# Optimization experiments

Measured on AMD Instinct MI355X. Metric: run time of the kernel, lower is better.

The kernel has to match this reference:

```python
import jax, jax.numpy as jnp
import numpy as np

B = 8192
N_IN = 1024
N_OUT = 1024
IN_OUT = N_IN + N_OUT


def setup_inputs() -> dict:
    key = jax.random.key(0)
    ks = jax.random.split(key, 11)
    s = 1.0 / np.sqrt(IN_OUT)  # nn.Linear default init scale
    inp = {
        "x": jax.random.normal(ks[0], (B, N_IN), dtype=jnp.float32),
        "out_tm1": jax.random.normal(ks[1], (B, N_OUT), dtype=jnp.float32),
        "state_tm1": jax.random.normal(ks[2], (B, N_OUT), dtype=jnp.float32),
        "Wf": jax.random.uniform(ks[3], (IN_OUT, N_OUT), jnp.float32, -s, s),
        "bf": jax.random.uniform(ks[4], (N_OUT,), jnp.float32, -s, s),
        "Wi": jax.random.uniform(ks[5], (IN_OUT, N_OUT), jnp.float32, -s, s),
        "bi": jax.random.uniform(ks[6], (N_OUT,), jnp.float32, -s, s),
        "Wc": jax.random.uniform(ks[7], (IN_OUT, N_OUT), jnp.float32, -s, s),
        "bc": jax.random.uniform(ks[8], (N_OUT,), jnp.float32, -s, s),
        "Wo": jax.random.uniform(ks[9], (IN_OUT, N_OUT), jnp.float32, -s, s),
        "bo": jax.random.uniform(ks[10], (N_OUT,), jnp.float32, -s, s),
    }
    return inp


def reference(x, out_tm1, state_tm1, Wf, bf, Wi, bi, Wc, bc, Wo, bo):
    xh = jnp.concatenate((x, out_tm1), axis=-1)  # [B, n_in+n_out]
    f = jax.nn.sigmoid(xh @ Wf + bf)             # forget gate
    i = jax.nn.sigmoid(xh @ Wi + bi)             # input gate
    c = jnp.tanh(xh @ Wc + bc)                   # candidates
    o = jax.nn.sigmoid(xh @ Wo + bo)             # output gate
    new_state = state_tm1 * f + i * c
    output_t = o * jnp.tanh(new_state)
    return (output_t, new_state)
```

## Files before the change

### kernel.cpp

```cpp
#include <hip/hip_runtime.h>

#define B_DIM 8192
#define NIN   1024
#define NOUT  1024
#define KDIM  2048

#define BM 128
#define BN 64
#define BK 64

typedef __bf16 bf16x8 __attribute__((ext_vector_type(8)));
typedef float  f32x4  __attribute__((ext_vector_type(4)));

__device__ __forceinline__ unsigned short f2bf(float f) {
  unsigned int u = __float_as_uint(f);
  u += 0x7fff + ((u >> 16) & 1);
  return (unsigned short)(u >> 16);
}

__device__ __forceinline__ float sigmoid_f(float x) {
  return 1.0f / (1.0f + __expf(-x));
}
__device__ __forceinline__ float tanh_f(float x) {
  return 1.0f - 2.0f / (__expf(2.0f * x) + 1.0f);
}

__device__ __forceinline__ void gload_lds16(const void* g, void* l) {
  __builtin_amdgcn_global_load_lds(
      (const __attribute__((address_space(1))) void*)g,
      (__attribute__((address_space(3))) void*)l, 16, 0, 0);
}

__global__ void pack_xh_kernel(const float* __restrict__ x,
                               const float* __restrict__ h,
                               unsigned short* __restrict__ xh) {
  const long total = (long)B_DIM * KDIM / 4;
  for (long i = (long)blockIdx.x * blockDim.x + threadIdx.x; i < total;
       i += (long)gridDim.x * blockDim.x) {
    long e = i * 4;
    int b = (int)(e >> 11);
    int c = (int)(e & 2047);
    float4 v = (c < NIN)
        ? *reinterpret_cast<const float4*>(x + (long)b * NIN + c)
        : *reinterpret_cast<const float4*>(h + (long)b * NOUT + (c - NIN));
    ushort4 o;
    o.x = f2bf(v.x); o.y = f2bf(v.y); o.z = f2bf(v.z); o.w = f2bf(v.w);
    *reinterpret_cast<ushort4*>(xh + e) = o;
  }
}

__global__ void transpose_w_kernel(const float* __restrict__ Wf,
                                   const float* __restrict__ Wi,
                                   const float* __restrict__ Wc,
                                   const float* __restrict__ Wo,
                                   unsigned short* __restrict__ wt) {
  __shared__ float tile[32][33];
  const int g = blockIdx.z;
  const float* W = (g == 0) ? Wf : (g == 1) ? Wi : (g == 2) ? Wc : Wo;
  const int n0 = blockIdx.x * 32;
  const int k0 = blockIdx.y * 32;
  const int tx = threadIdx.x, ty = threadIdx.y;
#pragma unroll
  for (int r = ty; r < 32; r += 8)
    tile[r][tx] = W[(long)(k0 + r) * NOUT + n0 + tx];
  __syncthreads();
  unsigned short* dst = wt + (long)g * NOUT * KDIM;
#pragma unroll
  for (int r = ty; r < 32; r += 8)
    dst[(long)(n0 + r) * KDIM + k0 + tx] = f2bf(tile[tx][r]);
}

__global__ __launch_bounds__(256, 2)
void lstm_gemm_kernel(const unsigned short* __restrict__ xh,
                      const unsigned short* __restrict__ wt,
                      const float* __restrict__ state,
                      const float* __restrict__ bfp,
                      const float* __restrict__ bip,
                      const float* __restrict__ bcp,
                      const float* __restrict__ bop,
                      float* __restrict__ out) {
  __shared__ __attribute__((aligned(16))) unsigned short lds_a[BM * BK];
  __shared__ __attribute__((aligned(16))) unsigned short lds_b[4][BN * BK];

  const int tid  = threadIdx.x;
  const int wave = tid >> 6;
  const int lane = tid & 63;
  const int m0 = blockIdx.y * BM;
  const int n0 = blockIdx.x * BN;
  const int wm = wave >> 1;
  const int wn = wave & 1;

  f32x4 acc[4][2][4];
#pragma unroll
  for (int mi = 0; mi < 4; ++mi)
#pragma unroll
    for (int ni = 0; ni < 2; ++ni)
#pragma unroll
      for (int g = 0; g < 4; ++g)
        acc[mi][ni][g] = (f32x4){0.f, 0.f, 0.f, 0.f};

  const char* xh_b = (const char*)xh;
  const char* wt_b = (const char*)wt;

  for (int kt = 0; kt < KDIM / BK; ++kt) {
#pragma unroll
    for (int j = 0; j < 4; ++j) {
      int off  = (wave * 4 + j) * 1024 + lane * 16;
      int row  = off >> 7;
      int colb = off & 127;
      gload_lds16(xh_b + ((long)(m0 + row) * 4096 + kt * 128 + colb),
                  (char*)lds_a + (wave * 4 + j) * 1024);
    }
#pragma unroll
    for (int j = 0; j < 8; ++j) {
      int off  = j * 1024 + lane * 16;
      int row  = off >> 7;
      int colb = off & 127;
      gload_lds16(wt_b + ((long)wave * 4194304 +
                          (long)(n0 + row) * 4096 + kt * 128 + colb),
                  (char*)lds_b + wave * 8192 + j * 1024);
    }
    __syncthreads();

#pragma unroll
    for (int s = 0; s < 2; ++s) {
      const int kb = s * 32 + (lane >> 4) * 8;
      bf16x8 af[4];
#pragma unroll
      for (int mi = 0; mi < 4; ++mi)
        af[mi] = *reinterpret_cast<const bf16x8*>(
            lds_a + (wm * 64 + mi * 16 + (lane & 15)) * BK + kb);
#pragma unroll
      for (int g = 0; g < 4; ++g) {
#pragma unroll
        for (int ni = 0; ni < 2; ++ni) {
          bf16x8 bfr = *reinterpret_cast<const bf16x8*>(
              lds_b[g] + (wn * 32 + ni * 16 + (lane & 15)) * BK + kb);
#pragma unroll
          for (int mi = 0; mi < 4; ++mi)
            acc[mi][ni][g] = __builtin_amdgcn_mfma_f32_16x16x32_bf16(
                af[mi], bfr, acc[mi][ni][g], 0, 0, 0);
        }
      }
    }
    __syncthreads();
  }

  const int colbase = n0 + wn * 32 + (lane & 15);
  const int rowbase = m0 + wm * 64 + ((lane >> 4) << 2);
#pragma unroll
  for (int ni = 0; ni < 2; ++ni) {
    const int c = colbase + ni * 16;
    const float bfv = bfp[c], biv = bip[c], bcv = bcp[c], bov = bop[c];
#pragma unroll
    for (int mi = 0; mi < 4; ++mi) {
      const int r0 = rowbase + mi * 16;
#pragma unroll
      for (int r = 0; r < 4; ++r) {
        const long row = r0 + r;
        float fg = sigmoid_f(acc[mi][ni][0][r] + bfv);
        float ig = sigmoid_f(acc[mi][ni][1][r] + biv);
        float cg = tanh_f(acc[mi][ni][2][r] + bcv);
        float og = sigmoid_f(acc[mi][ni][3][r] + bov);
        float st = state[row * NOUT + c];
        float ns = st * fg + ig * cg;
        out[row * NOUT + c] = og * tanh_f(ns);
        out[(long)B_DIM * NOUT + row * NOUT + c] = ns;
      }
    }
  }
}

extern "C" void kernel_launch(void* const* d_in, const int* in_sizes, int n_in,
                              void* d_out, int out_size, void* d_ws, size_t ws_size,
                              hipStream_t stream) {
  const float* x     = (const float*)d_in[0];
  const float* h     = (const float*)d_in[1];
  const float* state = (const float*)d_in[2];
  const float* Wf    = (const float*)d_in[3];
  const float* bfp   = (const float*)d_in[4];
  const float* Wi    = (const float*)d_in[5];
  const float* bip   = (const float*)d_in[6];
  const float* Wc    = (const float*)d_in[7];
  const float* bcp   = (const float*)d_in[8];
  const float* Wo    = (const float*)d_in[9];
  const float* bop   = (const float*)d_in[10];
  float* out = (float*)d_out;

  unsigned short* xh = (unsigned short*)d_ws;
  unsigned short* wt = (unsigned short*)((char*)d_ws +
                        (size_t)B_DIM * KDIM * 2);

  hipLaunchKernelGGL(pack_xh_kernel, dim3(2048), dim3(256), 0, stream,
                     x, h, xh);
  hipLaunchKernelGGL(transpose_w_kernel, dim3(NOUT / 32, KDIM / 32, 4),
                     dim3(32, 8), 0, stream, Wf, Wi, Wc, Wo, wt);
  hipLaunchKernelGGL(lstm_gemm_kernel, dim3(NOUT / BN, B_DIM / BM),
                     dim3(256), 0, stream,
                     xh, wt, state, bfp, bip, bcp, bop, out);
}
```

Measured before the change: 179.5 us.

## Rewrite LSTM GEMM as 256x256 tiled, double-buffered, swizzled 8-wave pipeline

```diff
diff --git a/kernel.cpp b/kernel.cpp
--- a/kernel.cpp
+++ b/kernel.cpp
@@ -1,13 +1,9 @@
 #include <hip/hip_runtime.h>
 
 #define B_DIM 8192
-#define NIN   1024
 #define NOUT  1024
 #define KDIM  2048
-
-#define BM 128
-#define BN 64
-#define BK 64
+#define NCI   4096
 
 typedef __bf16 bf16x8 __attribute__((ext_vector_type(8)));
 typedef float  f32x4  __attribute__((ext_vector_type(4)));
@@ -17,18 +13,21 @@
   u += 0x7fff + ((u >> 16) & 1);
   return (unsigned short)(u >> 16);
 }
-
 __device__ __forceinline__ float sigmoid_f(float x) {
   return 1.0f / (1.0f + __expf(-x));
 }
 __device__ __forceinline__ float tanh_f(float x) {
   return 1.0f - 2.0f / (__expf(2.0f * x) + 1.0f);
 }
-
 __device__ __forceinline__ void gload_lds16(const void* g, void* l) {
   __builtin_amdgcn_global_load_lds(
       (const __attribute__((address_space(1))) void*)g,
       (__attribute__((address_space(3))) void*)l, 16, 0, 0);
+}
+
+__device__ __forceinline__ int cimap(int g, int n) {
+  return ((n >> 6) << 8) | ((g >> 1) << 7) | (((n >> 4) & 3) << 5) |
+         ((g & 1) << 4) | (n & 15);
 }
 
 __global__ void pack_xh_kernel(const float* __restrict__ x,
@@ -40,9 +39,9 @@
     long e = i * 4;
     int b = (int)(e >> 11);
     int c = (int)(e & 2047);
-    float4 v = (c < NIN)
-        ? *reinterpret_cast<const float4*>(x + (long)b * NIN + c)
-        : *reinterpret_cast<const float4*>(h + (long)b * NOUT + (c - NIN));
+    float4 v = (c < 1024)
+        ? *reinterpret_cast<const float4*>(x + (long)b * 1024 + c)
+        : *reinterpret_cast<const float4*>(h + (long)b * 1024 + (c - 1024));
     ushort4 o;
     o.x = f2bf(v.x); o.y = f2bf(v.y); o.z = f2bf(v.z); o.w = f2bf(v.w);
     *reinterpret_cast<ushort4*>(xh + e) = o;
@@ -64,13 +63,54 @@
   for (int r = ty; r < 32; r += 8)
     tile[r][tx] = W[(long)(k0 + r) * NOUT + n0 + tx];
   __syncthreads();
-  unsigned short* dst = wt + (long)g * NOUT * KDIM;
-#pragma unroll
-  for (int r = ty; r < 32; r += 8)
-    dst[(long)(n0 + r) * KDIM + k0 + tx] = f2bf(tile[tx][r]);
-}
-
-__global__ __launch_bounds__(256, 2)
+#pragma unroll
+  for (int r = ty; r < 32; r += 8) {
+    int ci = cimap(g, n0 + r);
+    wt[(long)ci * KDIM + k0 + tx] = f2bf(tile[tx][r]);
+  }
+}
+
+#define BAR()   { __builtin_amdgcn_s_barrier(); __builtin_amdgcn_sched_barrier(0); }
+#define LGKM0() asm volatile("s_waitcnt lgkmcnt(0)" ::: "memory")
+#define VM4()   asm volatile("s_waitcnt vmcnt(4)" ::: "memory")
+#define VM0()   asm volatile("s_waitcnt vmcnt(0)" ::: "memory")
+
+__device__ __forceinline__ void stage_half(const char* g, long grow0, int kt,
+                                           char* ldsm, int base,
+                                           int wave, int lane) {
+  const int rsub = lane >> 3;
+  const int scol = (((lane & 7) ^ rsub) << 4);
+  const long rowb = (grow0 + wave * 8 + rsub) * 4096 + (long)kt * 128 + scol;
+  gload_lds16(g + rowb,               ldsm + base + wave * 1024);
+  gload_lds16(g + rowb + 64L * 4096,  ldsm + base + 8192 + wave * 1024);
+}
+
+#define LOAD_A(BUF, MQ)                                                     \
+  _Pragma("unroll") for (int mi = 0; mi < 4; ++mi) {                        \
+    const char* p_ = lds + (BUF)*32768 + (MQ)*16384 +                       \
+                     (wm * 64 + mi * 16 + lrow) * 128;                      \
+    af[mi][0] = *reinterpret_cast<const bf16x8*>(p_ + colA0);               \
+    af[mi][1] = *reinterpret_cast<const bf16x8*>(p_ + colA1);               \
+  }
+
+#define LOAD_B(BUF, NQ)                                                     \
+  _Pragma("unroll") for (int ni = 0; ni < 2; ++ni) {                        \
+    const char* p_ = lds + 65536 + (BUF)*32768 + (NQ)*16384 +               \
+                     (wn * 32 + ni * 16 + lrow) * 128;                      \
+    bq[ni][0] = *reinterpret_cast<const bf16x8*>(p_ + colA0);               \
+    bq[ni][1] = *reinterpret_cast<const bf16x8*>(p_ + colA1);               \
+  }
+
+#define MFMA16(MQ, NQ)                                                     \
+  __builtin_amdgcn_s_setprio(1);                                            \
+  _Pragma("unroll") for (int mi = 0; mi < 4; ++mi)                          \
+  _Pragma("unroll") for (int ni = 0; ni < 2; ++ni)                          \
+  _Pragma("unroll") for (int s = 0; s < 2; ++s)                             \
+    acc[MQ][NQ][mi][ni] = __builtin_amdgcn_mfma_f32_16x16x32_bf16(          \
+        af[mi][s], bq[ni][s], acc[MQ][NQ][mi][ni], 0, 0, 0);                \
+  __builtin_amdgcn_s_setprio(0);
+
+__global__ __launch_bounds__(512, 2)
 void lstm_gemm_kernel(const unsigned short* __restrict__ xh,
                       const unsigned short* __restrict__ wt,
                       const float* __restrict__ state,
@@ -79,96 +119,98 @@
                       const float* __restrict__ bcp,
                       const float* __restrict__ bop,
                       float* __restrict__ out) {
-  __shared__ __attribute__((aligned(16))) unsigned short lds_a[BM * BK];
-  __shared__ __attribute__((aligned(16))) unsigned short lds_b[4][BN * BK];
+  __shared__ __attribute__((aligned(128))) char lds[131072];
 
   const int tid  = threadIdx.x;
   const int wave = tid >> 6;
   const int lane = tid & 63;
-  const int m0 = blockIdx.y * BM;
-  const int n0 = blockIdx.x * BN;
-  const int wm = wave >> 1;
-  const int wn = wave & 1;
-
-  f32x4 acc[4][2][4];
-#pragma unroll
-  for (int mi = 0; mi < 4; ++mi)
-#pragma unroll
-    for (int ni = 0; ni < 2; ++ni)
-#pragma unroll
-      for (int g = 0; g < 4; ++g)
-        acc[mi][ni][g] = (f32x4){0.f, 0.f, 0.f, 0.f};
+  const int wm = wave >> 2;
+  const int wn = wave & 3;
+
+  int wg = blockIdx.y * 16 + blockIdx.x;
+  wg = (wg & 7) * 64 + (wg >> 3);
+  const int  bm = wg >> 4;
+  const int  bn = wg & 15;
+  const long m0 = (long)bm * 256;
+  const long n0 = (long)bn * 256;
+
+  const int lrow  = lane & 15;
+  const int csw   = (lane & 7) << 4;
+  const int ck    = (lane >> 4) << 4;
+  const int colA0 = ck ^ csw;
+  const int colA1 = (64 | ck) ^ csw;
 
   const char* xh_b = (const char*)xh;
   const char* wt_b = (const char*)wt;
 
-  for (int kt = 0; kt < KDIM / BK; ++kt) {
-#pragma unroll
-    for (int j = 0; j < 4; ++j) {
-      int off  = (wave * 4 + j) * 1024 + lane * 16;
-      int row  = off >> 7;
-      int colb = off & 127;
-      gload_lds16(xh_b + ((long)(m0 + row) * 4096 + kt * 128 + colb),
-                  (char*)lds_a + (wave * 4 + j) * 1024);
-    }
-#pragma unroll
-    for (int j = 0; j < 8; ++j) {
-      int off  = j * 1024 + lane * 16;
-      int row  = off >> 7;
-      int colb = off & 127;
-      gload_lds16(wt_b + ((long)wave * 4194304 +
-                          (long)(n0 + row) * 4096 + kt * 128 + colb),
-                  (char*)lds_b + wave * 8192 + j * 1024);
-    }
-    __syncthreads();
-
-#pragma unroll
-    for (int s = 0; s < 2; ++s) {
-      const int kb = s * 32 + (lane >> 4) * 8;
-      bf16x8 af[4];
-#pragma unroll
-      for (int mi = 0; mi < 4; ++mi)
-        af[mi] = *reinterpret_cast<const bf16x8*>(
-            lds_a + (wm * 64 + mi * 16 + (lane & 15)) * BK + kb);
-#pragma unroll
-      for (int g = 0; g < 4; ++g) {
-#pragma unroll
-        for (int ni = 0; ni < 2; ++ni) {
-          bf16x8 bfr = *reinterpret_cast<const bf16x8*>(
-              lds_b[g] + (wn * 32 + ni * 16 + (lane & 15)) * BK + kb);
-#pragma unroll
-          for (int mi = 0; mi < 4; ++mi)
-            acc[mi][ni][g] = __builtin_amdgcn_mfma_f32_16x16x32_bf16(
-                af[mi], bfr, acc[mi][ni][g], 0, 0, 0);
-        }
+  stage_half(xh_b, m0,        0, lds, 0,             wave, lane);
+  stage_half(xh_b, m0 + 128,  0, lds, 16384,         wave, lane);
+  stage_half(wt_b, n0,        0, lds, 65536,         wave, lane);
+  stage_half(wt_b, n0 + 128,  0, lds, 65536 + 16384, wave, lane);
+  stage_half(xh_b, m0,        1, lds, 32768,         wave, lane);
+  stage_half(wt_b, n0 + 128,  1, lds, 65536 + 32768 + 16384, wave, lane);
+
+  f32x4 acc[2][2][4][2] = {};
+  bf16x8 af[4][2];
+  bf16x8 bq[2][2];
+
+  VM4();
+  BAR();
+
+  for (int t = 0; t < 32; t += 2) {
+    const int k1 = (t + 1 <= 31) ? t + 1 : 31;
+    const int k2 = (t + 2 <= 31) ? t + 2 : 31;
+    const int k3 = (t + 3 <= 31) ? t + 3 : 31;
+
+    LOAD_A(0, 0) LOAD_B(0, 0)
+    stage_half(xh_b, m0 + 128, k1, lds, 32768 + 16384, wave, lane);
+    BAR(); LGKM0(); MFMA16(0, 0) BAR();
+    LOAD_B(0, 1)
+    stage_half(wt_b, n0, k1, lds, 65536 + 32768, wave, lane);
+    BAR(); LGKM0(); MFMA16(0, 1) BAR();
+    LOAD_A(0, 1)
+    stage_half(xh_b, m0, k2, lds, 0, wave, lane);
+    BAR(); LGKM0(); MFMA16(1, 1) BAR();
+    LOAD_B(0, 0)
+    stage_half(wt_b, n0 + 128, k2, lds, 65536 + 16384, wave, lane);
+    BAR(); LGKM0(); MFMA16(1, 0) VM4(); BAR();
+
+    LOAD_A(1, 0) LOAD_B(1, 0)
+    stage_half(xh_b, m0 + 128, k2, lds, 16384, wave, lane);
+    BAR(); LGKM0(); MFMA16(0, 0) BAR();
+    LOAD_B(1, 1)
+    stage_half(wt_b, n0, k2, lds, 65536, wave, lane);
+    BAR(); LGKM0(); MFMA16(0, 1) BAR();
+    LOAD_A(1, 1)
+    stage_half(xh_b, m0, k3, lds, 32768, wave, lane);
+    BAR(); LGKM0(); MFMA16(1, 1) BAR();
+    LOAD_B(1, 0)
+    stage_half(wt_b, n0 + 128, k3, lds, 65536 + 32768 + 16384, wave, lane);
+    BAR(); LGKM0(); MFMA16(1, 0) VM4(); BAR();
+  }
+  VM0();
+
+  const int   nout = bn * 64 + wn * 16 + lrow;
+  const int   rsub4 = (lane >> 4) << 2;
+  const float bfv = bfp[nout], biv = bip[nout];
+  const float bcv = bcp[nout], bov = bop[nout];
+  float* out2 = out + (long)B_DIM * NOUT;
+#pragma unroll
+  for (int mq = 0; mq < 2; ++mq)
+#pragma unroll
+    for (int mi = 0; mi < 4; ++mi)
+#pragma unroll
+      for (int v = 0; v < 4; ++v) {
+        const long row = m0 + mq * 128 + wm * 64 + mi * 16 + rsub4 + v;
+        float fg = sigmoid_f(acc[mq][0][mi][0][v] + bfv);
+        float ig = sigmoid_f(acc[mq][0][mi][1][v] + biv);
+        float cg = tanh_f   (acc[mq][1][mi][0][v] + bcv);
+        float og = sigmoid_f(acc[mq][1][mi][1][v] + bov);
+        float st = state[row * NOUT + nout];
+        float ns = st * fg + ig * cg;
+        out [row * NOUT + nout] = og * tanh_f(ns);
+        out2[row * NOUT + nout] = ns;
       }
-    }
-    __syncthreads();
-  }
-
-  const int colbase = n0 + wn * 32 + (lane & 15);
-  const int rowbase = m0 + wm * 64 + ((lane >> 4) << 2);
-#pragma unroll
-  for (int ni = 0; ni < 2; ++ni) {
-    const int c = colbase + ni * 16;
-    const float bfv = bfp[c], biv = bip[c], bcv = bcp[c], bov = bop[c];
-#pragma unroll
-    for (int mi = 0; mi < 4; ++mi) {
-      const int r0 = rowbase + mi * 16;
-#pragma unroll
-      for (int r = 0; r < 4; ++r) {
-        const long row = r0 + r;
-        float fg = sigmoid_f(acc[mi][ni][0][r] + bfv);
-        float ig = sigmoid_f(acc[mi][ni][1][r] + biv);
-        float cg = tanh_f(acc[mi][ni][2][r] + bcv);
-        float og = sigmoid_f(acc[mi][ni][3][r] + bov);
-        float st = state[row * NOUT + c];
-        float ns = st * fg + ig * cg;
-        out[row * NOUT + c] = og * tanh_f(ns);
-        out[(long)B_DIM * NOUT + row * NOUT + c] = ns;
-      }
-    }
-  }
 }
 
 extern "C" void kernel_launch(void* const* d_in, const int* in_sizes, int n_in,
@@ -188,14 +230,11 @@
   float* out = (float*)d_out;
 
   unsigned short* xh = (unsigned short*)d_ws;
-  unsigned short* wt = (unsigned short*)((char*)d_ws +
-                        (size_t)B_DIM * KDIM * 2);
-
-  hipLaunchKernelGGL(pack_xh_kernel, dim3(2048), dim3(256), 0, stream,
-                     x, h, xh);
+  unsigned short* wt = (unsigned short*)((char*)d_ws + (size_t)B_DIM * KDIM * 2);
+
+  hipLaunchKernelGGL(pack_xh_kernel, dim3(2048), dim3(256), 0, stream, x, h, xh);
   hipLaunchKernelGGL(transpose_w_kernel, dim3(NOUT / 32, KDIM / 32, 4),
                      dim3(32, 8), 0, stream, Wf, Wi, Wc, Wo, wt);
-  hipLaunchKernelGGL(lstm_gemm_kernel, dim3(NOUT / BN, B_DIM / BM),
-                     dim3(256), 0, stream,
+  hipLaunchKernelGGL(lstm_gemm_kernel, dim3(16, 32), dim3(512), 0, stream,
                      xh, wt, state, bfp, bip, bcp, bop, out);
 }
```

Measured after the change: 158.1 us. 1.13x faster.
